# Performance work log

Hardware: AMD Instinct MI355X
Metric: run time of the kernel (lower is better)

## Reference

```python
import jax, jax.numpy as jnp
import numpy as np

BN, N, M, P_OBS = 65536, 15, 6, 6

def _spd(k, b, n, scale=0.1):
    L = scale * jax.random.normal(k, (b, n, n), dtype=jnp.float32)
    return L @ L.mT + 0.1 * jnp.eye(n, dtype=jnp.float32)

def setup_inputs() -> dict:
    key = jax.random.key(0)
    ks = jax.random.split(key, 12)
    I_n = jnp.eye(N, dtype=jnp.float32)
    state = jax.random.normal(ks[0], (BN, N), dtype=jnp.float32)
    obs = jax.random.normal(ks[1], (BN, P_OBS), dtype=jnp.float32)
    u = jax.random.normal(ks[2], (BN, M), dtype=jnp.float32)
    P = _spd(ks[3], BN, N)
    A = I_n + 0.01 * jax.random.normal(ks[4], (BN, N, N), dtype=jnp.float32)
    B_mat = 0.1 * jax.random.normal(ks[5], (BN, N, M), dtype=jnp.float32)
    C = 0.1 * jax.random.normal(ks[6], (BN, P_OBS, N), dtype=jnp.float32)
    D = 0.1 * jax.random.normal(ks[7], (BN, P_OBS, M), dtype=jnp.float32)
    c1 = jax.random.normal(ks[8], (BN, N), dtype=jnp.float32)
    c2 = jax.random.normal(ks[9], (BN, P_OBS), dtype=jnp.float32)
    Q = _spd(ks[10], BN, M)
    R = _spd(ks[11], BN, P_OBS)
    return {"state": state, "obs": obs, "u": u, "P": P, "A": A, "B_mat": B_mat,
            "C": C, "D": D, "c1": c1, "c2": c2, "Q": Q, "R": R}

def reference(state, obs, u, P, A, B_mat, C, D, c1, c2, Q, R):
    # Linearized system: f(x,u) = A x + B u + c1 ; g(x,u) = C x + D u + c2
    I = jnp.eye(P.shape[-1], dtype=P.dtype)
    # priori state: xp = f(state, u)
    xp = jnp.einsum('bij,bj->bi', A, state) + jnp.einsum('bij,bj->bi', B_mat, u) + c1
    # priori covariance: P- = A P A^T + B Q B^T
    Pp = A @ P @ A.mT + B_mat @ Q @ B_mat.mT
    # Kalman gain: K = P- C^T pinv(C P- C^T + R)
    S = C @ Pp @ C.mT + R                       # [B, p, p]
    K = Pp @ C.mT @ jnp.linalg.pinv(S)          # [B, n, p]
    # innovation: e = obs - g(state, u)  (observation at previous state, as in source)
    e = obs - (jnp.einsum('bij,bj->bi', C, state) + jnp.einsum('bij,bj->bi', D, u) + c2)
    xp = xp + jnp.einsum('bij,bj->bi', K, e)
    # Joseph-form posterior covariance
    IKC = I - K @ C
    Pn = IKC @ Pp @ IKC.mT + K @ R @ K.mT
    return xp, Pn
```

## Files before the change

### kernel.cpp

```cpp
#include <hip/hip_runtime.h>

#define XOR16(v)     __shfl_xor((v), 16, 64)
#define FENCE() asm volatile("" ::: "memory")
#define SB() __builtin_amdgcn_sched_barrier(0)

#define STR    1932
#define OFF_M1    0
#define OFF_M2  320
#define OFF_C   620
#define OFF_S4  716
#define OFF_R   836
#define OFF_VX  884
#define OFF_VU  900
#define OFF_GB  908
#define OFF_HB  1228
#define OFF_SS  1868

using bf16x8 = __attribute__((ext_vector_type(8))) short;
using f32x4  = __attribute__((ext_vector_type(4))) float;

__device__ __forceinline__ unsigned short f2bf(float f) {
    union { float f; unsigned u; } v; v.f = f;
    unsigned r = v.u + 0x7FFFu + ((v.u >> 16) & 1u);
    return (unsigned short)(r >> 16);
}
__device__ __forceinline__ float dot8(const float* Lr, const float* v) {
    float4 x0 = *(const float4*)(Lr);
    float4 x1 = *(const float4*)(Lr + 4);
    return v[0]*x0.x + v[1]*x0.y + v[2]*x0.z + v[3]*x0.w
         + v[4]*x1.x + v[5]*x1.y + v[6]*x1.z + v[7]*x1.w;
}
__device__ __forceinline__ void rd8(const float* Lr, float* v) {
    float4 x0 = *(const float4*)(Lr);
    float4 x1 = *(const float4*)(Lr + 4);
    v[0]=x0.x; v[1]=x0.y; v[2]=x0.z; v[3]=x0.w;
    v[4]=x1.x; v[5]=x1.y; v[6]=x1.z; v[7]=x1.w;
}
__device__ __forceinline__ float dot6(const float* Lr, const float* v) {
    float4 x0 = *(const float4*)(Lr);
    float2 x1 = *(const float2*)(Lr + 4);
    return v[0]*x0.x + v[1]*x0.y + v[2]*x0.z + v[3]*x0.w + v[4]*x1.x + v[5]*x1.y;
}
__device__ __forceinline__ void rd6(const float* Lr, float* v) {
    float4 x0 = *(const float4*)(Lr);
    float2 x1 = *(const float2*)(Lr + 4);
    v[0]=x0.x; v[1]=x0.y; v[2]=x0.z; v[3]=x0.w; v[4]=x1.x; v[5]=x1.y;
}
__device__ __forceinline__ void wrow6(float* Lr, const float* v) {
    *(float4*)(Lr)     = make_float4(v[0],v[1],v[2],v[3]);
    *(float2*)(Lr + 4) = make_float2(v[4],v[5]);
}
__device__ __forceinline__ void wrow8(float* Lr, const float* v) {
    *(float4*)(Lr)     = make_float4(v[0],v[1],v[2],v[3]);
    *(float4*)(Lr + 4) = make_float4(v[4],v[5],v[6],v[7]);
}

__global__
__attribute__((amdgpu_flat_work_group_size(64, 64)))
__attribute__((amdgpu_waves_per_eu(2, 4)))
void ekf_kernel(
    const float* __restrict__ g_state, const float* __restrict__ g_obs,
    const float* __restrict__ g_u,     const float* __restrict__ g_P,
    const float* __restrict__ g_A,     const float* __restrict__ g_B,
    const float* __restrict__ g_C,     const float* __restrict__ g_D,
    const float* __restrict__ g_c1,    const float* __restrict__ g_c2,
    const float* __restrict__ g_Q,     const float* __restrict__ g_R,
    float* __restrict__ o_xp, float* __restrict__ o_Pn, int bn)
{
    __shared__ __align__(16) float lds[2 * STR];
    const int tid = threadIdx.x;
    const int ib0 = blockIdx.x * 2;
    const int nIt = min(2, bn - ib0);

    const int g   = tid >> 5;
    const int s   = tid & 31;
    const int r   = s & 15;
    const int h   = s >> 4;
    const int j0  = 8 * h;
    const int itc = ib0 + ((g < nIt) ? g : (nIt - 1));
    const int rc  = r < 15 ? r : 14;
    const int rc6 = r < 6 ? r : 5;
    float* L = lds + g * STR;

    const float* gp = g_P + (size_t)ib0 * 225;
    const float* ga = g_A + (size_t)ib0 * 225;
    const float* gc = g_C + (size_t)ib0 * 90;
    const float* gb = g_B + (size_t)ib0 * 90;
    const float* gq = g_Q + (size_t)ib0 * 36;
    const float* gr = g_R + (size_t)ib0 * 36;
    const float* gs = g_state + (size_t)ib0 * 15;
    const float* gu = g_u + (size_t)ib0 * 6;
    const int limPA = nIt * 225, limCB = nIt * 90, limQR = nIt * 36;
    const int limS = nIt * 15, limU = nIt * 6;

    float vP[8], vA[8], vC[3], vB[3], vQ[2], vR[2], vS, vU;
    #pragma unroll
    for (int t = 0; t < 8; ++t) {
        int i = min(tid + t * 64, limPA - 1);
        vP[t] = gp[i]; vA[t] = ga[i];
    }
    #pragma unroll
    for (int t = 0; t < 3; ++t) {
        int i = min(tid + t * 64, limCB - 1);
        vC[t] = gc[i]; vB[t] = gb[i];
    }
    #pragma unroll
    for (int t = 0; t < 2; ++t) {
        int i = min(tid + t * 64, limQR - 1);
        vQ[t] = gq[i]; vR[t] = gr[i];
    }
    vS = gs[min(tid, limS - 1)];
    vU = gu[min(tid, limU - 1)];
    float c1v  = g_c1[(size_t)itc * 15 + rc];
    float obsv = g_obs[(size_t)itc * 6 + rc6];
    float c2v  = g_c2[(size_t)itc * 6 + rc6];
    const float* Db = g_D + (size_t)itc * 36 + rc6 * 6;
    float dd0 = Db[0], dd1 = Db[1], dd2 = Db[2], dd3 = Db[3], dd4 = Db[4], dd5 = Db[5];

    #pragma unroll
    for (int g2 = 0; g2 < 2; ++g2) {
        #pragma unroll
        for (int t = 0; t < 4; ++t)
            *(float4*)(lds + g2 * STR + OFF_GB + t * 256 + tid * 4)
                = make_float4(0.f, 0.f, 0.f, 0.f);
    }
    FENCE();

    #pragma unroll
    for (int t = 0; t < 8; ++t) {
        int i = tid + t * 64;
        if (i < 450) {
            int it = i / 225, idx = i - it * 225;
            int rw = idx / 15, j = idx - rw * 15;
            lds[it * STR + OFF_M2 + rw * 20 + j] = vA[t];
        }
    }
    #pragma unroll
    for (int t = 0; t < 3; ++t) {
        int i = tid + t * 64;
        if (i < 180) {
            int it = i / 90, idx = i - it * 90;
            int rw = idx / 15, j = idx - rw * 15;
            lds[it * STR + OFF_C + rw * 16 + j] = vC[t];
            int rb = idx / 6, jb = idx - rb * 6;
            lds[it * STR + OFF_S4 + rb * 8 + jb] = vB[t];
        }
    }
    #pragma unroll
    for (int t = 0; t < 2; ++t) {
        int i = tid + t * 64;
        if (i < 72) {
            int it = i / 36, idx = i - it * 36;
            int rw = idx / 6, j = idx - rw * 6;
            lds[it * STR + OFF_R + rw * 8 + j] = vR[t];
        }
    }
    if (tid < 30) { int it = tid / 15, rw = tid - it * 15; lds[it * STR + OFF_VX + rw] = vS; }
    if (tid < 12) { int it = tid / 6,  rw = tid - it * 6;  lds[it * STR + OFF_VU + rw] = vU; }
    if (s < 6)  L[OFF_C + s * 16 + 15] = 0.f;
    if (s == 15) L[OFF_VX + 15] = 0.f;

    {
        unsigned short* lb = (unsigned short*)lds;
        #pragma unroll
        for (int t = 0; t < 8; ++t) {
            int i = tid + t * 64;
            if (i < 450) {
                int it = i / 225, idx = i - it * 225;
                int rw = idx / 15, j = idx - rw * 15;
                lb[(it * STR + OFF_GB) * 2 + rw * 40 + j] = f2bf(vA[t]);
                lb[(it * STR + OFF_HB) * 2 + rw * 40 + j] = f2bf(vP[t]);
            }
        }
        #pragma unroll
        for (int t = 0; t < 3; ++t) {
            int i = tid + t * 64;
            if (i < 180) {
                int it = i / 90, idx = i - it * 90;
                int rb = idx / 6, jb = idx - rb * 6;
                lb[(it * STR + OFF_GB) * 2 + rb * 40 + 16 + jb] = f2bf(vB[t]);
            }
        }
        #pragma unroll
        for (int t = 0; t < 2; ++t) {
            int i = tid + t * 64;
            if (i < 72) {
                int it = i / 36, idx = i - it * 36;
                int rq = idx / 6, cq = idx - rq * 6;
                lb[(it * STR + OFF_HB) * 2 + (16 + rq) * 40 + 16 + cq] = f2bf(vQ[t]);
            }
        }
    }
    FENCE(); SB();

    float xp;
    {
        float xh[8]; rd8(L + OFF_VX + j0, xh);
        float u6[6]; rd6(L + OFF_VU, u6);
        float xpp =  dot8(L + OFF_M2 + rc * 20 + j0, xh);
        float evp = -dot8(L + OFF_C + rc6 * 16 + j0, xh);
        if (h == 0) {
            xpp += c1v + dot6(L + OFF_S4 + rc * 8, u6);
            evp += obsv - c2v
                 - (dd0*u6[0] + dd1*u6[1] + dd2*u6[2]
                  + dd3*u6[3] + dd4*u6[4] + dd5*u6[5]);
        }
        xp = xpp + XOR16(xpp);
        float ev = evp + XOR16(evp);
        FENCE();
        if (h == 0 && r < 6) L[OFF_VX + r] = ev;
        FENCE();
    }

    const int q  = tid >> 4;
    const int cL = tid & 15;
    {
        char* lb = (char*)lds;
        bf16x8 ga0 = *(bf16x8*)(lb + (0*STR + OFF_GB)*4 + cL*80 + q*16);
        bf16x8 ga1 = *(bf16x8*)(lb + (1*STR + OFF_GB)*4 + cL*80 + q*16);
        bf16x8 ht0 = *(bf16x8*)(lb + (0*STR + OFF_HB)*4 + cL*80 + q*16);
        bf16x8 hb0 = *(bf16x8*)(lb + (0*STR + OFF_HB)*4 + (16+cL)*80 + q*16);
        bf16x8 ht1 = *(bf16x8*)(lb + (1*STR + OFF_HB)*4 + cL*80 + q*16);
        bf16x8 hb1 = *(bf16x8*)(lb + (1*STR + OFF_HB)*4 + (16+cL)*80 + q*16);
        f32x4 z = {0.f, 0.f, 0.f, 0.f};
        f32x4 zt0 = __builtin_amdgcn_mfma_f32_16x16x32_bf16(ht0, ga0, z, 0, 0, 0);
        f32x4 zb0 = __builtin_amdgcn_mfma_f32_16x16x32_bf16(hb0, ga0, z, 0, 0, 0);
        f32x4 zt1 = __builtin_amdgcn_mfma_f32_16x16x32_bf16(ht1, ga1, z, 0, 0, 0);
        f32x4 zb1 = __builtin_amdgcn_mfma_f32_16x16x32_bf16(hb1, ga1, z, 0, 0, 0);
        FENCE();
        {
            unsigned t0 = (unsigned)f2bf(zt0[0]) | ((unsigned)f2bf(zt0[1]) << 16);
            unsigned t1 = (unsigned)f2bf(zt0[2]) | ((unsigned)f2bf(zt0[3]) << 16);
            unsigned b0 = (unsigned)f2bf(zb0[0]) | ((unsigned)f2bf(zb0[1]) << 16);
            unsigned b1 = (unsigned)f2bf(zb0[2]) | ((unsigned)f2bf(zb0[3]) << 16);
            *(uint2*)(lb + (0*STR + OFF_HB)*4 + cL*80 + 8*q)      = make_uint2(t0, t1);
            *(uint2*)(lb + (0*STR + OFF_HB)*4 + cL*80 + 32 + 8*q) = make_uint2(b0, b1);
            unsigned u0 = (unsigned)f2bf(zt1[0]) | ((unsigned)f2bf(zt1[1]) << 16);
            unsigned u1 = (unsigned)f2bf(zt1[2]) | ((unsigned)f2bf(zt1[3]) << 16);
            unsigned v0 = (unsigned)f2bf(zb1[0]) | ((unsigned)f2bf(zb1[1]) << 16);
            unsigned v1 = (unsigned)f2bf(zb1[2]) | ((unsigned)f2bf(zb1[3]) << 16);
            *(uint2*)(lb + (1*STR + OFF_HB)*4 + cL*80 + 8*q)      = make_uint2(u0, u1);
            *(uint2*)(lb + (1*STR + OFF_HB)*4 + cL*80 + 32 + 8*q) = make_uint2(v0, v1);
        }
        FENCE(); SB();
        bf16x8 w0 = *(bf16x8*)(lb + (0*STR + OFF_HB)*4 + cL*80 + 16*q);
        bf16x8 w1 = *(bf16x8*)(lb + (1*STR + OFF_HB)*4 + cL*80 + 16*q);
        f32x4 pp0 = __builtin_amdgcn_mfma_f32_16x16x32_bf16(ga0, w0, z, 0, 0, 0);
        f32x4 pp1 = __builtin_amdgcn_mfma_f32_16x16x32_bf16(ga1, w1, z, 0, 0, 0);
        FENCE();
        *(f32x4*)(lds + 0*STR + OFF_M1 + cL*20 + 4*q) = pp0;
        *(f32x4*)(lds + 1*STR + OFF_M1 + cL*20 + 4*q) = pp1;
        FENCE(); SB();
    }

    float pp8[8];
    rd8(L + OFF_M1 + rc * 20 + j0, pp8);
    float ppct[6];
    {
        #define PCJ(c) ppct[(c)] = dot8(L + OFF_C + (c)*16 + j0, pp8)
        PCJ(0); PCJ(1); PCJ(2); PCJ(3); PCJ(4); PCJ(5);
        #pragma unroll
        for (int c = 0; c < 6; ++c) ppct[c] += XOR16(ppct[c]);
    }
    FENCE();
    if (h == 0 && r < 15) wrow6(L + OFF_M2 + r * 20, ppct);
    FENCE();

    float kk[6];
    {
        float sm[6];
        #pragma unroll
        for (int c = 0; c < 6; ++c) sm[c] = 0.f;
        {
            float ch[8]; rd8(L + OFF_C + rc6 * 16 + j0, ch);
            #define SAK(k) do { float pr[6]; rd6(L + OFF_M2 + min(j0 + (k), 14)*20, pr); \
                float cv = ch[(k)]; \
                sm[0]+=cv*pr[0]; sm[1]+=cv*pr[1]; sm[2]+=cv*pr[2]; \
                sm[3]+=cv*pr[3]; sm[4]+=cv*pr[4]; sm[5]+=cv*pr[5]; } while(0)
            SAK(0); SAK(1); SAK(2); SAK(3);
            SAK(4); SAK(5); SAK(6); SAK(7);
        }
        #pragma unroll
        for (int c = 0; c < 6; ++c) sm[c] += XOR16(sm[c]);
        if (h == 0 && r < 6) {
            float rr6[6]; rd6(L + OFF_R + r * 8, rr6);
            float srow[6];
            #pragma unroll
            for (int c = 0; c < 6; ++c) srow[c] = sm[c] + rr6[c];
            wrow6(L + OFF_SS + r * 8, srow);
        }
        FENCE();

        float r0[6], r1[6], r2[6], r3[6], r4[6], r5[6];
        rd6(L + OFF_SS + 0*8, r0); rd6(L + OFF_SS + 1*8, r1); rd6(L + OFF_SS + 2*8, r2);
        rd6(L + OFF_SS + 3*8, r3); rd6(L + OFF_SS + 4*8, r4); rd6(L + OFF_SS + 5*8, r5);

        float l00 = sqrtf(r0[0]);                 float i0 = 1.f / l00;
        float l10 = r1[0]*i0, l20 = r2[0]*i0, l30 = r3[0]*i0, l40 = r4[0]*i0, l50 = r5[0]*i0;
        float l11 = sqrtf(r1[1] - l10*l10);       float i1 = 1.f / l11;
        float l21 = (r2[1] - l20*l10)*i1;
        float l31 = (r3[1] - l30*l10)*i1;
        float l41 = (r4[1] - l40*l10)*i1;
        float l51 = (r5[1] - l50*l10)*i1;
        float l22 = sqrtf(r2[2] - l20*l20 - l21*l21); float i2 = 1.f / l22;
        float l32 = (r3[2] - l30*l20 - l31*l21)*i2;
        float l42 = (r4[2] - l40*l20 - l41*l21)*i2;
        float l52 = (r5[2] - l50*l20 - l51*l21)*i2;
        float l33 = sqrtf(r3[3] - l30*l30 - l31*l31 - l32*l32); float i3 = 1.f / l33;
        float l43 = (r4[3] - l40*l30 - l41*l31 - l42*l32)*i3;
        float l53 = (r5[3] - l50*l30 - l51*l31 - l52*l32)*i3;
        float l44 = sqrtf(r4[4] - l40*l40 - l41*l41 - l42*l42 - l43*l43); float i4 = 1.f / l44;
        float l54 = (r5[4] - l50*l40 - l51*l41 - l52*l42 - l53*l43)*i4;
        float l55 = sqrtf(r5[5] - l50*l50 - l51*l51 - l52*l52 - l53*l53 - l54*l54);
        float i5 = 1.f / l55;

        float y0 =  ppct[0]*i0;
        float y1 = (ppct[1] - l10*y0)*i1;
        float y2 = (ppct[2] - l20*y0 - l21*y1)*i2;
        float y3 = (ppct[3] - l30*y0 - l31*y1 - l32*y2)*i3;
        float y4 = (ppct[4] - l40*y0 - l41*y1 - l42*y2 - l43*y3)*i4;
        float y5 = (ppct[5] - l50*y0 - l51*y1 - l52*y2 - l53*y3 - l54*y4)*i5;
        kk[5] =  y5*i5;
        kk[4] = (y4 - l54*kk[5])*i4;
        kk[3] = (y3 - l43*kk[4] - l53*kk[5])*i3;
        kk[2] = (y2 - l32*kk[3] - l42*kk[4] - l52*kk[5])*i2;
        kk[1] = (y1 - l21*kk[2] - l31*kk[3] - l41*kk[4] - l51*kk[5])*i1;
        kk[0] = (y0 - l10*kk[1] - l20*kk[2] - l30*kk[3] - l40*kk[4] - l50*kk[5])*i0;
    }
    FENCE();
    if (h == 0 && r < 15) wrow6(L + OFF_M2 + r * 20 + 8, kk);
    FENCE();
    {
        float e6[6]; rd6(L + OFF_VX, e6);
        xp += kk[0]*e6[0] + kk[1]*e6[1] + kk[2]*e6[2]
            + kk[3]*e6[3] + kk[4]*e6[4] + kk[5]*e6[5];
    }

    float pn8[8];
    {
        float t38[8];
        #define T3J(j) do { float pr[6]; rd6(L + OFF_M2 + min(j0 + (j), 14)*20, pr); \
            t38[(j)] = pp8[(j)] - (kk[0]*pr[0]+kk[1]*pr[1]+kk[2]*pr[2] \
                                  +kk[3]*pr[3]+kk[4]*pr[4]+kk[5]*pr[5]); } while(0)
        T3J(0); T3J(1); T3J(2); T3J(3);
        T3J(4); T3J(5); T3J(6); T3J(7);
        if (j0 + 7 >= 15) t38[7] = 0.f;

        float w[6];
        #define GJ(c) w[(c)] = dot8(L + OFF_C + (c)*16 + j0, t38)
        GJ(0); GJ(1); GJ(2); GJ(3); GJ(4); GJ(5);
        #pragma unroll
        for (int c = 0; c < 6; ++c) w[c] = -(w[c] + XOR16(w[c]));

        #define KRK(k) do { float rk[6]; rd6(L + OFF_R + (k)*8, rk); \
            w[0]+=kk[(k)]*rk[0]; w[1]+=kk[(k)]*rk[1]; w[2]+=kk[(k)]*rk[2]; \
            w[3]+=kk[(k)]*rk[3]; w[4]+=kk[(k)]*rk[4]; w[5]+=kk[(k)]*rk[5]; } while(0)
        KRK(0); KRK(1); KRK(2); KRK(3); KRK(4); KRK(5);

        #define PNJ(j) do { float krow[6]; rd6(L + OFF_M2 + min(j0 + (j), 14)*20 + 8, krow); \
            pn8[(j)] = t38[(j)] + (w[0]*krow[0]+w[1]*krow[1]+w[2]*krow[2] \
                                  +w[3]*krow[3]+w[4]*krow[4]+w[5]*krow[5]); } while(0)
        PNJ(0); PNJ(1); PNJ(2); PNJ(3);
        PNJ(4); PNJ(5); PNJ(6); PNJ(7);
        if (j0 + 7 >= 15) pn8[7] = 0.f;
    }

    FENCE();
    if (r < 15) {
        wrow8(L + OFF_M1 + rc * 20 + j0, pn8);
        if (h == 0) L[OFF_S4 + r * 8 + 6] = xp;
    }
    FENCE();

    {
        float* gpn = o_Pn + (size_t)ib0 * 225;
        float sP[8];
        #pragma unroll
        for (int t = 0; t < 8; ++t) {
            int i = min(tid + t * 64, 449);
            int it = i / 225, idx = i - it * 225;
            int rw = idx / 15, j = idx - rw * 15;
            sP[t] = lds[it * STR + OFF_M1 + rw * 20 + j];
        }
        #pragma unroll
        for (int t = 0; t < 8; ++t) {
            int i = tid + t * 64;
            if (i < limPA) gpn[i] = sP[t];
        }
        float* gxp = o_xp + (size_t)ib0 * 15;
        if (tid < limS) {
            int it = tid / 15, rw = tid - it * 15;
            gxp[tid] = lds[it * STR + OFF_S4 + rw * 8 + 6];
        }
    }
}

extern "C" void kernel_launch(void* const* d_in, const int* in_sizes, int n_in,
                              void* d_out, int out_size, void* d_ws, size_t ws_size,
                              hipStream_t stream) {
    const float* g_state = (const float*)d_in[0];
    const float* g_obs   = (const float*)d_in[1];
    const float* g_u     = (const float*)d_in[2];
    const float* g_P     = (const float*)d_in[3];
    const float* g_A     = (const float*)d_in[4];
    const float* g_B     = (const float*)d_in[5];
    const float* g_C     = (const float*)d_in[6];
    const float* g_D     = (const float*)d_in[7];
    const float* g_c1    = (const float*)d_in[8];
    const float* g_c2    = (const float*)d_in[9];
    const float* g_Q     = (const float*)d_in[10];
    const float* g_R     = (const float*)d_in[11];

    const int bn = in_sizes[0] / 15;
    float* o_xp = (float*)d_out;
    float* o_pn = o_xp + (size_t)bn * 15;

    const int blocks = (bn + 1) / 2;
    ekf_kernel<<<blocks, 64, 0, stream>>>(
        g_state, g_obs, g_u, g_P, g_A, g_B, g_C, g_D, g_c1, g_c2, g_Q, g_R,
        o_xp, o_pn, bn);
}
```

Baseline: 108.5 us.

## Store A, B, C, R and intermediate P·Cᵀ, S, K as bf16 in LDS

Drops the fp32 LDS copies of A, B, C and R and reads them from bf16-packed buffers, some of which already existed for the MFMA stage. The intermediates P·Cᵀ, S and K are now also written as packed bf16 rows and unpacked with shifts. This shrinks the per-item LDS stride, which cuts LDS stores and footprint and may raise occupancy. The cost is lower precision in the Kalman gain, the Cholesky factorisation of S and the Joseph update, which could hurt accuracy, plus extra unpack ALU work.

```diff
diff --git a/kernel.cpp b/kernel.cpp
--- a/kernel.cpp
+++ b/kernel.cpp
@@ -4,17 +4,17 @@
 #define FENCE() asm volatile("" ::: "memory")
 #define SB() __builtin_amdgcn_sched_barrier(0)
 
-#define STR    1932
+#define STR    1544
 #define OFF_M1    0
-#define OFF_M2  320
-#define OFF_C   620
-#define OFF_S4  716
-#define OFF_R   836
-#define OFF_VX  884
-#define OFF_VU  900
-#define OFF_GB  908
-#define OFF_HB  1228
-#define OFF_SS  1868
+#define OFF_PK  320
+#define OFF_KB  380
+#define OFF_SB  440
+#define OFF_RB  464
+#define OFF_VX  488
+#define OFF_VU  504
+#define OFF_CB  520
+#define OFF_GB  568
+#define OFF_HB  888
 
 using bf16x8 = __attribute__((ext_vector_type(8))) short;
 using f32x4  = __attribute__((ext_vector_type(4))) float;
@@ -24,11 +24,25 @@
     unsigned r = v.u + 0x7FFFu + ((v.u >> 16) & 1u);
     return (unsigned short)(r >> 16);
 }
-__device__ __forceinline__ float dot8(const float* Lr, const float* v) {
-    float4 x0 = *(const float4*)(Lr);
-    float4 x1 = *(const float4*)(Lr + 4);
-    return v[0]*x0.x + v[1]*x0.y + v[2]*x0.z + v[3]*x0.w
-         + v[4]*x1.x + v[5]*x1.y + v[6]*x1.z + v[7]*x1.w;
+__device__ __forceinline__ uint4 ldu4(const float* p) { return *(const uint4*)p; }
+__device__ __forceinline__ void unpk8(const uint4 u, float* v) {
+    v[0]=__uint_as_float(u.x<<16); v[1]=__uint_as_float(u.x&0xffff0000u);
+    v[2]=__uint_as_float(u.y<<16); v[3]=__uint_as_float(u.y&0xffff0000u);
+    v[4]=__uint_as_float(u.z<<16); v[5]=__uint_as_float(u.z&0xffff0000u);
+    v[6]=__uint_as_float(u.w<<16); v[7]=__uint_as_float(u.w&0xffff0000u);
+}
+__device__ __forceinline__ void unpk6(const uint4 u, float* v) {
+    v[0]=__uint_as_float(u.x<<16); v[1]=__uint_as_float(u.x&0xffff0000u);
+    v[2]=__uint_as_float(u.y<<16); v[3]=__uint_as_float(u.y&0xffff0000u);
+    v[4]=__uint_as_float(u.z<<16); v[5]=__uint_as_float(u.z&0xffff0000u);
+}
+__device__ __forceinline__ void wpk6(float* Lr, const float* v) {
+    uint4 u;
+    u.x = (unsigned)f2bf(v[0]) | ((unsigned)f2bf(v[1])<<16);
+    u.y = (unsigned)f2bf(v[2]) | ((unsigned)f2bf(v[3])<<16);
+    u.z = (unsigned)f2bf(v[4]) | ((unsigned)f2bf(v[5])<<16);
+    u.w = 0;
+    *(uint4*)Lr = u;
 }
 __device__ __forceinline__ void rd8(const float* Lr, float* v) {
     float4 x0 = *(const float4*)(Lr);
@@ -36,19 +50,10 @@
     v[0]=x0.x; v[1]=x0.y; v[2]=x0.z; v[3]=x0.w;
     v[4]=x1.x; v[5]=x1.y; v[6]=x1.z; v[7]=x1.w;
 }
-__device__ __forceinline__ float dot6(const float* Lr, const float* v) {
-    float4 x0 = *(const float4*)(Lr);
-    float2 x1 = *(const float2*)(Lr + 4);
-    return v[0]*x0.x + v[1]*x0.y + v[2]*x0.z + v[3]*x0.w + v[4]*x1.x + v[5]*x1.y;
-}
 __device__ __forceinline__ void rd6(const float* Lr, float* v) {
     float4 x0 = *(const float4*)(Lr);
     float2 x1 = *(const float2*)(Lr + 4);
     v[0]=x0.x; v[1]=x0.y; v[2]=x0.z; v[3]=x0.w; v[4]=x1.x; v[5]=x1.y;
-}
-__device__ __forceinline__ void wrow6(float* Lr, const float* v) {
-    *(float4*)(Lr)     = make_float4(v[0],v[1],v[2],v[3]);
-    *(float2*)(Lr + 4) = make_float2(v[4],v[5]);
 }
 __device__ __forceinline__ void wrow8(float* Lr, const float* v) {
     *(float4*)(Lr)     = make_float4(v[0],v[1],v[2],v[3]);
@@ -121,43 +126,13 @@
     for (int g2 = 0; g2 < 2; ++g2) {
         #pragma unroll
         for (int t = 0; t < 4; ++t)
-            *(float4*)(lds + g2 * STR + OFF_GB + t * 256 + tid * 4)
+            *(float4*)(lds + g2 * STR + OFF_CB + t * 256 + tid * 4)
                 = make_float4(0.f, 0.f, 0.f, 0.f);
     }
     FENCE();
 
-    #pragma unroll
-    for (int t = 0; t < 8; ++t) {
-        int i = tid + t * 64;
-        if (i < 450) {
-            int it = i / 225, idx = i - it * 225;
-            int rw = idx / 15, j = idx - rw * 15;
-            lds[it * STR + OFF_M2 + rw * 20 + j] = vA[t];
-        }
-    }
-    #pragma unroll
-    for (int t = 0; t < 3; ++t) {
-        int i = tid + t * 64;
-        if (i < 180) {
-            int it = i / 90, idx = i - it * 90;
-            int rw = idx / 15, j = idx - rw * 15;
-            lds[it * STR + OFF_C + rw * 16 + j] = vC[t];
-            int rb = idx / 6, jb = idx - rb * 6;
-            lds[it * STR + OFF_S4 + rb * 8 + jb] = vB[t];
-        }
-    }
-    #pragma unroll
-    for (int t = 0; t < 2; ++t) {
-        int i = tid + t * 64;
-        if (i < 72) {
-            int it = i / 36, idx = i - it * 36;
-            int rw = idx / 6, j = idx - rw * 6;
-            lds[it * STR + OFF_R + rw * 8 + j] = vR[t];
-        }
-    }
     if (tid < 30) { int it = tid / 15, rw = tid - it * 15; lds[it * STR + OFF_VX + rw] = vS; }
     if (tid < 12) { int it = tid / 6,  rw = tid - it * 6;  lds[it * STR + OFF_VU + rw] = vU; }
-    if (s < 6)  L[OFF_C + s * 16 + 15] = 0.f;
     if (s == 15) L[OFF_VX + 15] = 0.f;
 
     {
@@ -179,6 +154,8 @@
                 int it = i / 90, idx = i - it * 90;
                 int rb = idx / 6, jb = idx - rb * 6;
                 lb[(it * STR + OFF_GB) * 2 + rb * 40 + 16 + jb] = f2bf(vB[t]);
+                int rw = idx / 15, j = idx - rw * 15;
+                lb[(it * STR + OFF_CB) * 2 + rw * 16 + j] = f2bf(vC[t]);
             }
         }
         #pragma unroll
@@ -188,6 +165,7 @@
                 int it = i / 36, idx = i - it * 36;
                 int rq = idx / 6, cq = idx - rq * 6;
                 lb[(it * STR + OFF_HB) * 2 + (16 + rq) * 40 + 16 + cq] = f2bf(vQ[t]);
+                lb[(it * STR + OFF_RB) * 2 + rq * 8 + cq] = f2bf(vR[t]);
             }
         }
     }
@@ -197,10 +175,16 @@
     {
         float xh[8]; rd8(L + OFF_VX + j0, xh);
         float u6[6]; rd6(L + OFF_VU, u6);
-        float xpp =  dot8(L + OFF_M2 + rc * 20 + j0, xh);
-        float evp = -dot8(L + OFF_C + rc6 * 16 + j0, xh);
+        float ar[8]; unpk8(ldu4(L + OFF_GB + rc * 20 + 4 * h), ar);
+        float cr[8]; unpk8(ldu4(L + OFF_CB + rc6 * 8 + 4 * h), cr);
+        float xpp = ar[0]*xh[0]+ar[1]*xh[1]+ar[2]*xh[2]+ar[3]*xh[3]
+                  + ar[4]*xh[4]+ar[5]*xh[5]+ar[6]*xh[6]+ar[7]*xh[7];
+        float evp = -(cr[0]*xh[0]+cr[1]*xh[1]+cr[2]*xh[2]+cr[3]*xh[3]
+                    + cr[4]*xh[4]+cr[5]*xh[5]+cr[6]*xh[6]+cr[7]*xh[7]);
         if (h == 0) {
-            xpp += c1v + dot6(L + OFF_S4 + rc * 8, u6);
+            float br[6]; unpk6(ldu4(L + OFF_GB + rc * 20 + 8), br);
+            xpp += c1v + br[0]*u6[0]+br[1]*u6[1]+br[2]*u6[2]
+                       + br[3]*u6[3]+br[4]*u6[4]+br[5]*u6[5];
             evp += obsv - c2v
                  - (dd0*u6[0] + dd1*u6[1] + dd2*u6[2]
                   + dd3*u6[3] + dd4*u6[4] + dd5*u6[5]);
@@ -257,13 +241,15 @@
     rd8(L + OFF_M1 + rc * 20 + j0, pp8);
     float ppct[6];
     {
-        #define PCJ(c) ppct[(c)] = dot8(L + OFF_C + (c)*16 + j0, pp8)
+        #define PCJ(c) do { float cc[8]; unpk8(ldu4(L + OFF_CB + (c)*8 + 4*h), cc); \
+            ppct[(c)] = cc[0]*pp8[0]+cc[1]*pp8[1]+cc[2]*pp8[2]+cc[3]*pp8[3] \
+                      + cc[4]*pp8[4]+cc[5]*pp8[5]+cc[6]*pp8[6]+cc[7]*pp8[7]; } while(0)
         PCJ(0); PCJ(1); PCJ(2); PCJ(3); PCJ(4); PCJ(5);
         #pragma unroll
         for (int c = 0; c < 6; ++c) ppct[c] += XOR16(ppct[c]);
     }
     FENCE();
-    if (h == 0 && r < 15) wrow6(L + OFF_M2 + r * 20, ppct);
+    if (h == 0 && r < 15) wpk6(L + OFF_PK + 4 * r, ppct);
     FENCE();
 
     float kk[6];
@@ -272,8 +258,8 @@
         #pragma unroll
         for (int c = 0; c < 6; ++c) sm[c] = 0.f;
         {
-            float ch[8]; rd8(L + OFF_C + rc6 * 16 + j0, ch);
-            #define SAK(k) do { float pr[6]; rd6(L + OFF_M2 + min(j0 + (k), 14)*20, pr); \
+            float ch[8]; unpk8(ldu4(L + OFF_CB + rc6 * 8 + 4 * h), ch);
+            #define SAK(k) do { float pr[6]; unpk6(ldu4(L + OFF_PK + 4*min(j0 + (k), 14)), pr); \
                 float cv = ch[(k)]; \
                 sm[0]+=cv*pr[0]; sm[1]+=cv*pr[1]; sm[2]+=cv*pr[2]; \
                 sm[3]+=cv*pr[3]; sm[4]+=cv*pr[4]; sm[5]+=cv*pr[5]; } while(0)
@@ -283,17 +269,18 @@
         #pragma unroll
         for (int c = 0; c < 6; ++c) sm[c] += XOR16(sm[c]);
         if (h == 0 && r < 6) {
-            float rr6[6]; rd6(L + OFF_R + r * 8, rr6);
+            float rr6[6]; unpk6(ldu4(L + OFF_RB + 4 * r), rr6);
             float srow[6];
             #pragma unroll
             for (int c = 0; c < 6; ++c) srow[c] = sm[c] + rr6[c];
-            wrow6(L + OFF_SS + r * 8, srow);
+            wpk6(L + OFF_SB + 4 * r, srow);
         }
         FENCE();
 
         float r0[6], r1[6], r2[6], r3[6], r4[6], r5[6];
-        rd6(L + OFF_SS + 0*8, r0); rd6(L + OFF_SS + 1*8, r1); rd6(L + OFF_SS + 2*8, r2);
-        rd6(L + OFF_SS + 3*8, r3); rd6(L + OFF_SS + 4*8, r4); rd6(L + OFF_SS + 5*8, r5);
+        unpk6(ldu4(L + OFF_SB + 0),  r0); unpk6(ldu4(L + OFF_SB + 4),  r1);
+        unpk6(ldu4(L + OFF_SB + 8),  r2); unpk6(ldu4(L + OFF_SB + 12), r3);
+        unpk6(ldu4(L + OFF_SB + 16), r4); unpk6(ldu4(L + OFF_SB + 20), r5);
 
         float l00 = sqrtf(r0[0]);                 float i0 = 1.f / l00;
         float l10 = r1[0]*i0, l20 = r2[0]*i0, l30 = r3[0]*i0, l40 = r4[0]*i0, l50 = r5[0]*i0;
@@ -328,7 +315,7 @@
         kk[0] = (y0 - l10*kk[1] - l20*kk[2] - l30*kk[3] - l40*kk[4] - l50*kk[5])*i0;
     }
     FENCE();
-    if (h == 0 && r < 15) wrow6(L + OFF_M2 + r * 20 + 8, kk);
+    if (h == 0 && r < 15) wpk6(L + OFF_KB + 4 * r, kk);
     FENCE();
     {
         float e6[6]; rd6(L + OFF_VX, e6);
@@ -339,7 +326,7 @@
     float pn8[8];
     {
         float t38[8];
-        #define T3J(j) do { float pr[6]; rd6(L + OFF_M2 + min(j0 + (j), 14)*20, pr); \
+        #define T3J(j) do { float pr[6]; unpk6(ldu4(L + OFF_PK + 4*min(j0 + (j), 14)), pr); \
             t38[(j)] = pp8[(j)] - (kk[0]*pr[0]+kk[1]*pr[1]+kk[2]*pr[2] \
                                   +kk[3]*pr[3]+kk[4]*pr[4]+kk[5]*pr[5]); } while(0)
         T3J(0); T3J(1); T3J(2); T3J(3);
@@ -347,17 +334,19 @@
         if (j0 + 7 >= 15) t38[7] = 0.f;
 
         float w[6];
-        #define GJ(c) w[(c)] = dot8(L + OFF_C + (c)*16 + j0, t38)
+        #define GJ(c) do { float cc[8]; unpk8(ldu4(L + OFF_CB + (c)*8 + 4*h), cc); \
+            w[(c)] = cc[0]*t38[0]+cc[1]*t38[1]+cc[2]*t38[2]+cc[3]*t38[3] \
+                   + cc[4]*t38[4]+cc[5]*t38[5]+cc[6]*t38[6]+cc[7]*t38[7]; } while(0)
         GJ(0); GJ(1); GJ(2); GJ(3); GJ(4); GJ(5);
         #pragma unroll
         for (int c = 0; c < 6; ++c) w[c] = -(w[c] + XOR16(w[c]));
 
-        #define KRK(k) do { float rk[6]; rd6(L + OFF_R + (k)*8, rk); \
+        #define KRK(k) do { float rk[6]; unpk6(ldu4(L + OFF_RB + 4*(k)), rk); \
             w[0]+=kk[(k)]*rk[0]; w[1]+=kk[(k)]*rk[1]; w[2]+=kk[(k)]*rk[2]; \
             w[3]+=kk[(k)]*rk[3]; w[4]+=kk[(k)]*rk[4]; w[5]+=kk[(k)]*rk[5]; } while(0)
         KRK(0); KRK(1); KRK(2); KRK(3); KRK(4); KRK(5);
 
-        #define PNJ(j) do { float krow[6]; rd6(L + OFF_M2 + min(j0 + (j), 14)*20 + 8, krow); \
+        #define PNJ(j) do { float krow[6]; unpk6(ldu4(L + OFF_KB + 4*min(j0 + (j), 14)), krow); \
             pn8[(j)] = t38[(j)] + (w[0]*krow[0]+w[1]*krow[1]+w[2]*krow[2] \
                                   +w[3]*krow[3]+w[4]*krow[4]+w[5]*krow[5]); } while(0)
         PNJ(0); PNJ(1); PNJ(2); PNJ(3);
@@ -368,7 +357,7 @@
     FENCE();
     if (r < 15) {
         wrow8(L + OFF_M1 + rc * 20 + j0, pn8);
-        if (h == 0) L[OFF_S4 + r * 8 + 6] = xp;
+        if (h == 0) L[OFF_PK + 4 * r + 3] = xp;
     }
     FENCE();
 
@@ -390,7 +379,7 @@
         float* gxp = o_xp + (size_t)ib0 * 15;
         if (tid < limS) {
             int it = tid / 15, rw = tid - it * 15;
-            gxp[tid] = lds[it * STR + OFF_S4 + rw * 8 + 6];
+            gxp[tid] = lds[it * STR + OFF_PK + 4 * rw + 3];
         }
     }
 }
```

Result: faster. 100.7 us (-7.2%).
